# Performance work log

Hardware: AMD Instinct MI355X
Metric: run time of the kernel (lower is better)

Reference implementation:

```python
import jax, jax.numpy as jnp
import numpy as np

GRID = 32          # latent grid points per dim
N_OUT = 16384      # output query points
BATCH = 2
C = 256            # projection_channels (latent hidden width)
D = 3              # gno_coord_dim
OUT_CH = 4         # out_channels
RADIUS = 0.045     # gno_radius


def _radius_neighbors(x, y, r):
    """Radius ball search: for each query x_i find all y_j with ||x_i-y_j||<=r.
    Returns (nb_index, out_index) edge lists, sorted by query (CSR order)."""
    r2 = np.float32(r * r)
    nb_idx, out_idx = [], []
    for s in range(0, x.shape[0], 512):  # chunk to bound memory
        d2 = ((x[s:s + 512, None, :] - y[None, :, :]) ** 2).sum(-1)
        oi, yi = np.nonzero(d2 <= r2)
        out_idx.append((oi + s).astype(np.int32))
        nb_idx.append(yi.astype(np.int32))
    return np.concatenate(nb_idx), np.concatenate(out_idx)


def setup_inputs() -> dict:
    key = jax.random.key(0)
    ks = jax.random.split(key, 8)
    # latent queries: regular grid on [0,1]^3
    g = np.linspace(0.0, 1.0, GRID, dtype=np.float32)
    gx, gy, gz = np.meshgrid(g, g, g, indexing="ij")
    grid = np.stack([gx, gy, gz], axis=-1)               # (G,G,G,3)
    latent_queries = jnp.asarray(grid[None])             # (1,G,G,G,3)
    output_queries = jax.random.uniform(ks[0], (1, N_OUT, D), dtype=jnp.float32)
    nb_idx, out_idx = _radius_neighbors(np.asarray(output_queries[0]),
                                        grid.reshape(-1, D), RADIUS)
    latent_embed = jax.random.normal(ks[1], (BATCH, GRID, GRID, GRID, C), dtype=jnp.float32)

    def lin(k, fi, fo):
        kw, kb = jax.random.split(k)
        W = jax.random.normal(kw, (fi, fo), dtype=jnp.float32) / np.sqrt(fi).astype(np.float32)
        b = jax.random.normal(kb, (fo,), dtype=jnp.float32) * 0.01
        return W, b

    W1, b1 = lin(ks[2], 2 * D, 512)
    W2, b2 = lin(ks[3], 512, 256)
    W3, b3 = lin(ks[4], 256, C)
    Wp, bp = lin(ks[5], C, OUT_CH)
    return {"latent_embed": latent_embed, "latent_queries": latent_queries,
            "output_queries": output_queries,
            "nb_index": jnp.asarray(nb_idx), "out_index": jnp.asarray(out_idx),
            "W1": W1, "b1": b1, "W2": W2, "b2": b2, "W3": W3, "b3": b3,
            "Wp": Wp, "bp": bp}


def reference(latent_embed, latent_queries, output_queries, nb_index, out_index,
              W1, b1, W2, b2, W3, b3, Wp, bp):
    y = latent_queries[0].reshape(-1, latent_queries.shape[-1])   # (n_in, d) grid coords
    x = output_queries[0]                                         # (n_out, d)
    n_out = x.shape[0]
    b = latent_embed.shape[0]
    f_y = latent_embed.reshape(b, -1, latent_embed.shape[-1])     # (b, n_in, c)

    # per-edge kernel MLP on concat(y_j, x_i) -- 'linear' transform type
    agg = jnp.concatenate([y[nb_index], x[out_index]], axis=-1)   # (E, 2d)
    h = jax.nn.gelu(agg @ W1 + b1, approximate=False)             # (E, 512)
    h = jax.nn.gelu(h @ W2 + b2, approximate=False)               # (E, 256)
    k = h @ W3 + b3                                               # (E, c) kernel values

    # k(x_i, y_j) * f(y_j), then mean-reduce over each neighborhood
    msg = k[None, :, :] * f_y[:, nb_index, :]                     # (b, E, c)
    sums = jax.vmap(lambda m: jax.ops.segment_sum(m, out_index, num_segments=n_out))(msg)
    cnt = jax.ops.segment_sum(jnp.ones(nb_index.shape[0], dtype=k.dtype),
                              out_index, num_segments=n_out)
    mean = sums / jnp.maximum(cnt, 1.0)[None, :, None]            # (b, n_out, c)

    # pointwise projection (single Linear, no nonlinearity)
    return mean @ Wp + bp                                         # (b, n_out, out_ch)
```

## Files before the change

kernel.cpp:

```cpp
#include <hip/hip_runtime.h>
#include <math.h>

#define NGRID 32768
#define NOUT  16384
#define CCH   256
#define H1DIM 512
#define TE    32

typedef _Float16 f16x8 __attribute__((ext_vector_type(8)));
typedef float    f32x16 __attribute__((ext_vector_type(16)));

__device__ __forceinline__ unsigned short f32_to_f16_bits(float v) {
    _Float16 h = (_Float16)v;
    return __builtin_bit_cast(unsigned short, h);
}

__device__ __forceinline__ unsigned swz_row(int r) {
    return (unsigned)(((r & 7) ^ ((r >> 3) & 3)) << 4);
}

__device__ __forceinline__ float gelu_fast(float x) {
    float ax = fabsf(x) * 0.70710678118654752f;
    float t  = __builtin_amdgcn_rcpf(fmaf(0.3275911f, ax, 1.0f));
    float p  = fmaf(fmaf(fmaf(fmaf(1.061405429f, t, -1.453152027f), t, 1.421413741f), t,
                         -0.284496736f), t, 0.254829592f) * t;
    float e  = __expf(-ax * ax);
    float er = fmaf(-p, e, 1.0f);
    er = (x >= 0.0f) ? er : -er;
    return 0.5f * x * (1.0f + er);
}

__global__ __launch_bounds__(256) void gino_pack_kernel(
    const float* __restrict__ W2, const float* __restrict__ W3,
    unsigned short* __restrict__ W2F, unsigned short* __restrict__ W3F)
{
    int idx = blockIdx.x * 256 + threadIdx.x;
    if (idx < 32 * 8 * 64) {
        int l = idx & 63, g = (idx >> 6) & 7, ks = idx >> 9;
        int ch = g * 32 + (l & 31);
        int k0 = ks * 16 + (l >> 5) * 8;
        unsigned int u[4];
        #pragma unroll
        for (int p = 0; p < 4; ++p) {
            unsigned int lo = f32_to_f16_bits(W2[(k0 + 2 * p) * CCH + ch]);
            unsigned int hh = f32_to_f16_bits(W2[(k0 + 2 * p + 1) * CCH + ch]);
            u[p] = lo | (hh << 16);
        }
        *(uint4*)(W2F + idx * 8) = make_uint4(u[0], u[1], u[2], u[3]);
    } else if (idx < 32 * 8 * 64 + 16 * 8 * 64) {
        int i2 = idx - 32 * 8 * 64;
        int l = i2 & 63, g = (i2 >> 6) & 7, ks = i2 >> 9;
        int ch = g * 32 + (l & 31);
        int k0 = ks * 16 + (l >> 5) * 8;
        unsigned int u[4];
        #pragma unroll
        for (int p = 0; p < 4; ++p) {
            unsigned int lo = f32_to_f16_bits(W3[(k0 + 2 * p) * CCH + ch]);
            unsigned int hh = f32_to_f16_bits(W3[(k0 + 2 * p + 1) * CCH + ch]);
            u[p] = lo | (hh << 16);
        }
        *(uint4*)(W3F + i2 * 8) = make_uint4(u[0], u[1], u[2], u[3]);
    }
}

__global__ __launch_bounds__(256, 4) void gino_edge_kernel(
    const float* __restrict__ latent_embed,
    const float* __restrict__ latent_queries,
    const float* __restrict__ output_queries,
    const int*   __restrict__ nb_index,
    const int*   __restrict__ out_index,
    const float* __restrict__ W1, const float* __restrict__ b1,
    const float* __restrict__ b2, const float* __restrict__ b3,
    const unsigned short* __restrict__ W2F,
    const unsigned short* __restrict__ W3F,
    const float* __restrict__ Wp,
    float* __restrict__ sums, float* __restrict__ cnt, int E)
{
    __shared__ __align__(16) unsigned char s_h1[TE * 512];
    __shared__ __align__(16) unsigned char s_h2[TE * 512];
    __shared__ float s_agg[TE][8];
    __shared__ float s_pm[TE][8];
    __shared__ int s_nb[TE], s_oi[TE], s_valid[TE];

    const int tid = threadIdx.x;
    const int e0  = blockIdx.x * TE;

    ((float*)s_pm)[tid] = 0.0f;
    if (tid < TE) {
        int e     = e0 + tid;
        int valid = (e < E) ? 1 : 0;
        int ec    = valid ? e : (E - 1);
        int nb    = nb_index[ec];
        int oi    = out_index[ec];
        s_nb[tid] = nb; s_oi[tid] = oi; s_valid[tid] = valid;
        s_agg[tid][0] = latent_queries[nb * 3 + 0];
        s_agg[tid][1] = latent_queries[nb * 3 + 1];
        s_agg[tid][2] = latent_queries[nb * 3 + 2];
        s_agg[tid][3] = output_queries[oi * 3 + 0];
        s_agg[tid][4] = output_queries[oi * 3 + 1];
        s_agg[tid][5] = output_queries[oi * 3 + 2];
        if (valid) atomicAdd(&cnt[oi], 1.0f);
    }
    __syncthreads();

    const int l  = tid & 63;
    const int w  = tid >> 6;
    const int le = l & 31;
    const int hi = l >> 5;
    const unsigned swz = swz_row(le);

    f32x16 acc0 = {}, acc1 = {};

    #pragma unroll
    for (int chunk = 0; chunk < 2; ++chunk) {
        {
            const int kc = chunk * 256 + l * 4;
            float w1r[6][4];
            #pragma unroll
            for (int i = 0; i < 6; ++i)
                *(float4*)&w1r[i][0] = *(const float4*)(W1 + i * H1DIM + kc);
            float4 b1r = *(const float4*)(b1 + kc);
            #pragma unroll
            for (int ee = 0; ee < 8; ++ee) {
                int e = w * 8 + ee;
                float a0 = s_agg[e][0], a1 = s_agg[e][1], a2 = s_agg[e][2];
                float a3 = s_agg[e][3], a4 = s_agg[e][4], a5 = s_agg[e][5];
                unsigned int u[2];
                #pragma unroll
                for (int p = 0; p < 2; ++p) {
                    unsigned int uu[2];
                    #pragma unroll
                    for (int q = 0; q < 2; ++q) {
                        int j = 2 * p + q;
                        float v = (j == 0) ? b1r.x : (j == 1) ? b1r.y : (j == 2) ? b1r.z : b1r.w;
                        v = fmaf(a0, w1r[0][j], v);
                        v = fmaf(a1, w1r[1][j], v);
                        v = fmaf(a2, w1r[2][j], v);
                        v = fmaf(a3, w1r[3][j], v);
                        v = fmaf(a4, w1r[4][j], v);
                        v = fmaf(a5, w1r[5][j], v);
                        uu[q] = f32_to_f16_bits(gelu_fast(v));
                    }
                    u[p] = uu[0] | (uu[1] << 16);
                }
                *(uint2*)(s_h1 + e * 512 + (((unsigned)(l * 8)) ^ swz_row(e))) =
                    make_uint2(u[0], u[1]);
            }
        }
        __syncthreads();

        {
            const unsigned short* pa = W2F + (size_t)chunk * 16 * 4096 + w * 2 * 512 + l * 8;
            #pragma unroll
            for (int ks = 0; ks < 16; ++ks) {
                f16x8 bfr = *(const f16x8*)(s_h1 + le * 512 +
                              (((unsigned)(ks * 32 + hi * 16)) ^ swz));
                f16x8 a0 = *(const f16x8*)(pa + ks * 4096);
                f16x8 a1 = *(const f16x8*)(pa + ks * 4096 + 512);
                acc0 = __builtin_amdgcn_mfma_f32_32x32x16_f16(a0, bfr, acc0, 0, 0, 0);
                acc1 = __builtin_amdgcn_mfma_f32_32x32x16_f16(a1, bfr, acc1, 0, 0, 0);
            }
        }
        __syncthreads();
    }

    #pragma unroll
    for (int t2 = 0; t2 < 2; ++t2) {
        int g = w * 2 + t2;
        #pragma unroll
        for (int q = 0; q < 4; ++q) {
            int ch0 = g * 32 + q * 8 + hi * 4;
            float4 bb = *(const float4*)(b2 + ch0);
            float v0 = (t2 ? acc1[q * 4 + 0] : acc0[q * 4 + 0]) + bb.x;
            float v1 = (t2 ? acc1[q * 4 + 1] : acc0[q * 4 + 1]) + bb.y;
            float v2 = (t2 ? acc1[q * 4 + 2] : acc0[q * 4 + 2]) + bb.z;
            float v3 = (t2 ? acc1[q * 4 + 3] : acc0[q * 4 + 3]) + bb.w;
            unsigned int u0 = f32_to_f16_bits(gelu_fast(v0)) |
                              ((unsigned)f32_to_f16_bits(gelu_fast(v1)) << 16);
            unsigned int u1 = f32_to_f16_bits(gelu_fast(v2)) |
                              ((unsigned)f32_to_f16_bits(gelu_fast(v3)) << 16);
            *(uint2*)(s_h2 + le * 512 + (((unsigned)(ch0 * 2)) ^ swz)) = make_uint2(u0, u1);
        }
    }
    __syncthreads();

    f32x16 kc0 = {}, kc1 = {};
    {
        const unsigned short* pa = W3F + w * 2 * 512 + l * 8;
        #pragma unroll
        for (int ks = 0; ks < 16; ++ks) {
            f16x8 bfr = *(const f16x8*)(s_h2 + le * 512 +
                          (((unsigned)(ks * 32 + hi * 16)) ^ swz));
            f16x8 a0 = *(const f16x8*)(pa + ks * 4096);
            f16x8 a1 = *(const f16x8*)(pa + ks * 4096 + 512);
            kc0 = __builtin_amdgcn_mfma_f32_32x32x16_f16(a0, bfr, kc0, 0, 0, 0);
            kc1 = __builtin_amdgcn_mfma_f32_32x32x16_f16(a1, bfr, kc1, 0, 0, 0);
        }
    }

    {
        int nb = s_nb[le];
        const float* fb0 = latent_embed + (size_t)nb * CCH;
        const float* fb1 = latent_embed + ((size_t)NGRID + nb) * CCH;
        float pm00 = 0.f, pm01 = 0.f, pm02 = 0.f, pm03 = 0.f;
        float pm10 = 0.f, pm11 = 0.f, pm12 = 0.f, pm13 = 0.f;
        #pragma unroll
        for (int t2 = 0; t2 < 2; ++t2) {
            #pragma unroll
            for (int q = 0; q < 4; ++q) {
                int ch0 = (w * 2 + t2) * 32 + q * 8 + hi * 4;
                float4 bb = *(const float4*)(b3 + ch0);
                float kv0 = (t2 ? kc1[q * 4 + 0] : kc0[q * 4 + 0]) + bb.x;
                float kv1 = (t2 ? kc1[q * 4 + 1] : kc0[q * 4 + 1]) + bb.y;
                float kv2 = (t2 ? kc1[q * 4 + 2] : kc0[q * 4 + 2]) + bb.z;
                float kv3 = (t2 ? kc1[q * 4 + 3] : kc0[q * 4 + 3]) + bb.w;
                float4 f0 = *(const float4*)(fb0 + ch0);
                float4 f1 = *(const float4*)(fb1 + ch0);
                float4 wp0 = *(const float4*)(Wp + (ch0 + 0) * 4);
                float4 wp1 = *(const float4*)(Wp + (ch0 + 1) * 4);
                float4 wp2 = *(const float4*)(Wp + (ch0 + 2) * 4);
                float4 wp3 = *(const float4*)(Wp + (ch0 + 3) * 4);
                float t0 = kv0 * f0.x, t1 = kv1 * f0.y, t2v = kv2 * f0.z, t3 = kv3 * f0.w;
                pm00 = fmaf(t0, wp0.x, fmaf(t1, wp1.x, fmaf(t2v, wp2.x, fmaf(t3, wp3.x, pm00))));
                pm01 = fmaf(t0, wp0.y, fmaf(t1, wp1.y, fmaf(t2v, wp2.y, fmaf(t3, wp3.y, pm01))));
                pm02 = fmaf(t0, wp0.z, fmaf(t1, wp1.z, fmaf(t2v, wp2.z, fmaf(t3, wp3.z, pm02))));
                pm03 = fmaf(t0, wp0.w, fmaf(t1, wp1.w, fmaf(t2v, wp2.w, fmaf(t3, wp3.w, pm03))));
                float s0 = kv0 * f1.x, s1 = kv1 * f1.y, s2 = kv2 * f1.z, s3 = kv3 * f1.w;
                pm10 = fmaf(s0, wp0.x, fmaf(s1, wp1.x, fmaf(s2, wp2.x, fmaf(s3, wp3.x, pm10))));
                pm11 = fmaf(s0, wp0.y, fmaf(s1, wp1.y, fmaf(s2, wp2.y, fmaf(s3, wp3.y, pm11))));
                pm12 = fmaf(s0, wp0.z, fmaf(s1, wp1.z, fmaf(s2, wp2.z, fmaf(s3, wp3.z, pm12))));
                pm13 = fmaf(s0, wp0.w, fmaf(s1, wp1.w, fmaf(s2, wp2.w, fmaf(s3, wp3.w, pm13))));
            }
        }
        atomicAdd(&s_pm[le][0], pm00);
        atomicAdd(&s_pm[le][1], pm01);
        atomicAdd(&s_pm[le][2], pm02);
        atomicAdd(&s_pm[le][3], pm03);
        atomicAdd(&s_pm[le][4], pm10);
        atomicAdd(&s_pm[le][5], pm11);
        atomicAdd(&s_pm[le][6], pm12);
        atomicAdd(&s_pm[le][7], pm13);
    }
    __syncthreads();

    {
        int el = tid >> 3;
        int v  = tid & 7;
        if (s_valid[el]) {
            int b  = v >> 2;
            int oc = v & 3;
            atomicAdd(&sums[((size_t)b * NOUT + s_oi[el]) * 4 + oc], s_pm[el][v]);
        }
    }
}

__global__ __launch_bounds__(256) void gino_finalize_kernel(
    const float* __restrict__ sums,
    const float* __restrict__ cnt,
    const float* __restrict__ bp,
    float* __restrict__ out)
{
    int idx = blockIdx.x * 256 + threadIdx.x;
    if (idx >= 2 * NOUT * 4) return;
    int oc = idx & 3;
    int i  = (idx >> 2) & (NOUT - 1);
    float c = fmaxf(cnt[i], 1.0f);
    out[idx] = sums[idx] / c + bp[oc];
}

extern "C" void kernel_launch(void* const* d_in, const int* in_sizes, int n_in,
                              void* d_out, int out_size, void* d_ws, size_t ws_size,
                              hipStream_t stream) {
    const float* latent_embed   = (const float*)d_in[0];
    const float* latent_queries = (const float*)d_in[1];
    const float* output_queries = (const float*)d_in[2];
    const int*   nb_index       = (const int*)d_in[3];
    const int*   out_index      = (const int*)d_in[4];
    const float* W1 = (const float*)d_in[5];
    const float* b1 = (const float*)d_in[6];
    const float* W2 = (const float*)d_in[7];
    const float* b2 = (const float*)d_in[8];
    const float* W3 = (const float*)d_in[9];
    const float* b3 = (const float*)d_in[10];
    const float* Wp = (const float*)d_in[11];
    const float* bp = (const float*)d_in[12];

    const int E = in_sizes[3];

    float* sums = (float*)d_ws;
    float* cnt  = sums + 2 * NOUT * 4;
    unsigned short* W2F = (unsigned short*)(cnt + NOUT);
    unsigned short* W3F = W2F + 32 * 8 * 64 * 8;

    hipMemsetAsync(d_ws, 0, (size_t)(2 * NOUT * 4 + NOUT) * sizeof(float), stream);

    gino_pack_kernel<<<(32 * 8 * 64 + 16 * 8 * 64 + 255) / 256, 256, 0, stream>>>(
        W2, W3, W2F, W3F);

    int nblk = (E + TE - 1) / TE;
    gino_edge_kernel<<<nblk, 256, 0, stream>>>(
        latent_embed, latent_queries, output_queries, nb_index, out_index,
        W1, b1, b2, b3, W2F, W3F, Wp, sums, cnt, E);

    gino_finalize_kernel<<<(2 * NOUT * 4 + 255) / 256, 256, 0, stream>>>(
        sums, cnt, bp, (float*)d_out);
}
```

Baseline: 291.3 us.

## Double edge tile to 64 with 8 waves and software-pipeline MFMA operand loads

Each block now handles 64 edges with 512 threads (8 waves). Each wave owns 32 output channels, and its single weight fragment is reused across two 32-edge MFMA tiles, so each global weight load feeds twice as many edges. The MFMA loops prefetch the A and B fragments one or two k-steps ahead, and the projection partials are combined with a cross-half shuffle before the shared-memory atomics. The trade-off is more shared memory and registers per block, which may lower occupancy at the 4-blocks launch bound. The LDS swizzle is also simplified.

```diff
diff --git a/kernel.cpp b/kernel.cpp
--- a/kernel.cpp
+++ b/kernel.cpp
@@ -5,7 +5,8 @@
 #define NOUT  16384
 #define CCH   256
 #define H1DIM 512
-#define TE    32
+#define TE    64
+#define NTHR  512
 
 typedef _Float16 f16x8 __attribute__((ext_vector_type(8)));
 typedef float    f32x16 __attribute__((ext_vector_type(16)));
@@ -13,10 +14,6 @@
 __device__ __forceinline__ unsigned short f32_to_f16_bits(float v) {
     _Float16 h = (_Float16)v;
     return __builtin_bit_cast(unsigned short, h);
-}
-
-__device__ __forceinline__ unsigned swz_row(int r) {
-    return (unsigned)(((r & 7) ^ ((r >> 3) & 3)) << 4);
 }
 
 __device__ __forceinline__ float gelu_fast(float x) {
@@ -63,7 +60,7 @@
     }
 }
 
-__global__ __launch_bounds__(256, 4) void gino_edge_kernel(
+__global__ __launch_bounds__(NTHR, 4) void gino_edge_kernel(
     const float* __restrict__ latent_embed,
     const float* __restrict__ latent_queries,
     const float* __restrict__ output_queries,
@@ -107,7 +104,7 @@
     const int w  = tid >> 6;
     const int le = l & 31;
     const int hi = l >> 5;
-    const unsigned swz = swz_row(le);
+    const unsigned bswz = (unsigned)(le & 7) << 4;
 
     f32x16 acc0 = {}, acc1 = {};
 
@@ -143,103 +140,111 @@
                     }
                     u[p] = uu[0] | (uu[1] << 16);
                 }
-                *(uint2*)(s_h1 + e * 512 + (((unsigned)(l * 8)) ^ swz_row(e))) =
+                *(uint2*)(s_h1 + e * 512 + (((unsigned)(l * 8)) ^ (((unsigned)(ee & 7)) << 4))) =
                     make_uint2(u[0], u[1]);
             }
         }
         __syncthreads();
 
         {
-            const unsigned short* pa = W2F + (size_t)chunk * 16 * 4096 + w * 2 * 512 + l * 8;
+            const unsigned short* pa = W2F + (size_t)(chunk * 16) * 4096 + w * 512 + l * 8;
+            #define BRD1(t, ks) (*(const f16x8*)(s_h1 + ((t) * 32 + le) * 512 + \
+                                 (((unsigned)((ks) * 32 + hi * 16)) ^ bswz)))
+            f16x8 aC = *(const f16x8*)(pa);
+            f16x8 aN = *(const f16x8*)(pa + 4096);
+            f16x8 b0 = BRD1(0, 0), b1f = BRD1(1, 0);
             #pragma unroll
             for (int ks = 0; ks < 16; ++ks) {
-                f16x8 bfr = *(const f16x8*)(s_h1 + le * 512 +
-                              (((unsigned)(ks * 32 + hi * 16)) ^ swz));
-                f16x8 a0 = *(const f16x8*)(pa + ks * 4096);
-                f16x8 a1 = *(const f16x8*)(pa + ks * 4096 + 512);
-                acc0 = __builtin_amdgcn_mfma_f32_32x32x16_f16(a0, bfr, acc0, 0, 0, 0);
-                acc1 = __builtin_amdgcn_mfma_f32_32x32x16_f16(a1, bfr, acc1, 0, 0, 0);
+                f16x8 aNN = aN, bN0 = b0, bN1 = b1f;
+                if (ks < 14) aNN = *(const f16x8*)(pa + (size_t)(ks + 2) * 4096);
+                if (ks < 15) { bN0 = BRD1(0, ks + 1); bN1 = BRD1(1, ks + 1); }
+                acc0 = __builtin_amdgcn_mfma_f32_32x32x16_f16(aC, b0,  acc0, 0, 0, 0);
+                acc1 = __builtin_amdgcn_mfma_f32_32x32x16_f16(aC, b1f, acc1, 0, 0, 0);
+                aC = aN; aN = aNN; b0 = bN0; b1f = bN1;
             }
+            #undef BRD1
         }
         __syncthreads();
     }
 
     #pragma unroll
-    for (int t2 = 0; t2 < 2; ++t2) {
-        int g = w * 2 + t2;
+    for (int t = 0; t < 2; ++t) {
+        int erow = t * 32 + le;
         #pragma unroll
         for (int q = 0; q < 4; ++q) {
-            int ch0 = g * 32 + q * 8 + hi * 4;
+            int ch0 = w * 32 + q * 8 + hi * 4;
             float4 bb = *(const float4*)(b2 + ch0);
-            float v0 = (t2 ? acc1[q * 4 + 0] : acc0[q * 4 + 0]) + bb.x;
-            float v1 = (t2 ? acc1[q * 4 + 1] : acc0[q * 4 + 1]) + bb.y;
-            float v2 = (t2 ? acc1[q * 4 + 2] : acc0[q * 4 + 2]) + bb.z;
-            float v3 = (t2 ? acc1[q * 4 + 3] : acc0[q * 4 + 3]) + bb.w;
+            float v0 = (t ? acc1[q * 4 + 0] : acc0[q * 4 + 0]) + bb.x;
+            float v1 = (t ? acc1[q * 4 + 1] : acc0[q * 4 + 1]) + bb.y;
+            float v2 = (t ? acc1[q * 4 + 2] : acc0[q * 4 + 2]) + bb.z;
+            float v3 = (t ? acc1[q * 4 + 3] : acc0[q * 4 + 3]) + bb.w;
             unsigned int u0 = f32_to_f16_bits(gelu_fast(v0)) |
                               ((unsigned)f32_to_f16_bits(gelu_fast(v1)) << 16);
             unsigned int u1 = f32_to_f16_bits(gelu_fast(v2)) |
                               ((unsigned)f32_to_f16_bits(gelu_fast(v3)) << 16);
-            *(uint2*)(s_h2 + le * 512 + (((unsigned)(ch0 * 2)) ^ swz)) = make_uint2(u0, u1);
+            *(uint2*)(s_h2 + erow * 512 + (((unsigned)(ch0 * 2)) ^ bswz)) = make_uint2(u0, u1);
         }
     }
     __syncthreads();
 
     f32x16 kc0 = {}, kc1 = {};
     {
-        const unsigned short* pa = W3F + w * 2 * 512 + l * 8;
+        const unsigned short* pa = W3F + w * 512 + l * 8;
+        #define BRD2(t, ks) (*(const f16x8*)(s_h2 + ((t) * 32 + le) * 512 + \
+                             (((unsigned)((ks) * 32 + hi * 16)) ^ bswz)))
+        f16x8 aC = *(const f16x8*)(pa);
+        f16x8 aN = *(const f16x8*)(pa + 4096);
+        f16x8 b0 = BRD2(0, 0), b1f = BRD2(1, 0);
         #pragma unroll
         for (int ks = 0; ks < 16; ++ks) {
-            f16x8 bfr = *(const f16x8*)(s_h2 + le * 512 +
-                          (((unsigned)(ks * 32 + hi * 16)) ^ swz));
-            f16x8 a0 = *(const f16x8*)(pa + ks * 4096);
-            f16x8 a1 = *(const f16x8*)(pa + ks * 4096 + 512);
-            kc0 = __builtin_amdgcn_mfma_f32_32x32x16_f16(a0, bfr, kc0, 0, 0, 0);
-            kc1 = __builtin_amdgcn_mfma_f32_32x32x16_f16(a1, bfr, kc1, 0, 0, 0);
-        }
-    }
-
-    {
-        int nb = s_nb[le];
+            f16x8 aNN = aN, bN0 = b0, bN1 = b1f;
+            if (ks < 14) aNN = *(const f16x8*)(pa + (size_t)(ks + 2) * 4096);
+            if (ks < 15) { bN0 = BRD2(0, ks + 1); bN1 = BRD2(1, ks + 1); }
+            kc0 = __builtin_amdgcn_mfma_f32_32x32x16_f16(aC, b0,  kc0, 0, 0, 0);
+            kc1 = __builtin_amdgcn_mfma_f32_32x32x16_f16(aC, b1f, kc1, 0, 0, 0);
+            aC = aN; aN = aNN; b0 = bN0; b1f = bN1;
+        }
+        #undef BRD2
+    }
+
+    #pragma unroll
+    for (int t = 0; t < 2; ++t) {
+        int e  = t * 32 + le;
+        int nb = s_nb[e];
         const float* fb0 = latent_embed + (size_t)nb * CCH;
         const float* fb1 = latent_embed + ((size_t)NGRID + nb) * CCH;
-        float pm00 = 0.f, pm01 = 0.f, pm02 = 0.f, pm03 = 0.f;
-        float pm10 = 0.f, pm11 = 0.f, pm12 = 0.f, pm13 = 0.f;
-        #pragma unroll
-        for (int t2 = 0; t2 < 2; ++t2) {
+        float pm[8] = {0.f, 0.f, 0.f, 0.f, 0.f, 0.f, 0.f, 0.f};
+        #pragma unroll
+        for (int q = 0; q < 4; ++q) {
+            int ch0 = w * 32 + q * 8 + hi * 4;
+            float4 bb = *(const float4*)(b3 + ch0);
+            float kv0 = (t ? kc1[q * 4 + 0] : kc0[q * 4 + 0]) + bb.x;
+            float kv1 = (t ? kc1[q * 4 + 1] : kc0[q * 4 + 1]) + bb.y;
+            float kv2 = (t ? kc1[q * 4 + 2] : kc0[q * 4 + 2]) + bb.z;
+            float kv3 = (t ? kc1[q * 4 + 3] : kc0[q * 4 + 3]) + bb.w;
+            float4 f0 = *(const float4*)(fb0 + ch0);
+            float4 f1 = *(const float4*)(fb1 + ch0);
+            float4 wp0 = *(const float4*)(Wp + (ch0 + 0) * 4);
+            float4 wp1 = *(const float4*)(Wp + (ch0 + 1) * 4);
+            float4 wp2 = *(const float4*)(Wp + (ch0 + 2) * 4);
+            float4 wp3 = *(const float4*)(Wp + (ch0 + 3) * 4);
+            float t0 = kv0 * f0.x, t1 = kv1 * f0.y, t2v = kv2 * f0.z, t3 = kv3 * f0.w;
+            pm[0] = fmaf(t0, wp0.x, fmaf(t1, wp1.x, fmaf(t2v, wp2.x, fmaf(t3, wp3.x, pm[0]))));
+            pm[1] = fmaf(t0, wp0.y, fmaf(t1, wp1.y, fmaf(t2v, wp2.y, fmaf(t3, wp3.y, pm[1]))));
+            pm[2] = fmaf(t0, wp0.z, fmaf(t1, wp1.z, fmaf(t2v, wp2.z, fmaf(t3, wp3.z, pm[2]))));
+            pm[3] = fmaf(t0, wp0.w, fmaf(t1, wp1.w, fmaf(t2v, wp2.w, fmaf(t3, wp3.w, pm[3]))));
+            float s0 = kv0 * f1.x, s1 = kv1 * f1.y, s2 = kv2 * f1.z, s3 = kv3 * f1.w;
+            pm[4] = fmaf(s0, wp0.x, fmaf(s1, wp1.x, fmaf(s2, wp2.x, fmaf(s3, wp3.x, pm[4]))));
+            pm[5] = fmaf(s0, wp0.y, fmaf(s1, wp1.y, fmaf(s2, wp2.y, fmaf(s3, wp3.y, pm[5]))));
+            pm[6] = fmaf(s0, wp0.z, fmaf(s1, wp1.z, fmaf(s2, wp2.z, fmaf(s3, wp3.z, pm[6]))));
+            pm[7] = fmaf(s0, wp0.w, fmaf(s1, wp1.w, fmaf(s2, wp2.w, fmaf(s3, wp3.w, pm[7]))));
+        }
+        #pragma unroll
+        for (int v = 0; v < 8; ++v) pm[v] += __shfl_xor(pm[v], 32);
+        if (hi == 0) {
             #pragma unroll
-            for (int q = 0; q < 4; ++q) {
-                int ch0 = (w * 2 + t2) * 32 + q * 8 + hi * 4;
-                float4 bb = *(const float4*)(b3 + ch0);
-                float kv0 = (t2 ? kc1[q * 4 + 0] : kc0[q * 4 + 0]) + bb.x;
-                float kv1 = (t2 ? kc1[q * 4 + 1] : kc0[q * 4 + 1]) + bb.y;
-                float kv2 = (t2 ? kc1[q * 4 + 2] : kc0[q * 4 + 2]) + bb.z;
-                float kv3 = (t2 ? kc1[q * 4 + 3] : kc0[q * 4 + 3]) + bb.w;
-                float4 f0 = *(const float4*)(fb0 + ch0);
-                float4 f1 = *(const float4*)(fb1 + ch0);
-                float4 wp0 = *(const float4*)(Wp + (ch0 + 0) * 4);
-                float4 wp1 = *(const float4*)(Wp + (ch0 + 1) * 4);
-                float4 wp2 = *(const float4*)(Wp + (ch0 + 2) * 4);
-                float4 wp3 = *(const float4*)(Wp + (ch0 + 3) * 4);
-                float t0 = kv0 * f0.x, t1 = kv1 * f0.y, t2v = kv2 * f0.z, t3 = kv3 * f0.w;
-                pm00 = fmaf(t0, wp0.x, fmaf(t1, wp1.x, fmaf(t2v, wp2.x, fmaf(t3, wp3.x, pm00))));
-                pm01 = fmaf(t0, wp0.y, fmaf(t1, wp1.y, fmaf(t2v, wp2.y, fmaf(t3, wp3.y, pm01))));
-                pm02 = fmaf(t0, wp0.z, fmaf(t1, wp1.z, fmaf(t2v, wp2.z, fmaf(t3, wp3.z, pm02))));
-                pm03 = fmaf(t0, wp0.w, fmaf(t1, wp1.w, fmaf(t2v, wp2.w, fmaf(t3, wp3.w, pm03))));
-                float s0 = kv0 * f1.x, s1 = kv1 * f1.y, s2 = kv2 * f1.z, s3 = kv3 * f1.w;
-                pm10 = fmaf(s0, wp0.x, fmaf(s1, wp1.x, fmaf(s2, wp2.x, fmaf(s3, wp3.x, pm10))));
-                pm11 = fmaf(s0, wp0.y, fmaf(s1, wp1.y, fmaf(s2, wp2.y, fmaf(s3, wp3.y, pm11))));
-                pm12 = fmaf(s0, wp0.z, fmaf(s1, wp1.z, fmaf(s2, wp2.z, fmaf(s3, wp3.z, pm12))));
-                pm13 = fmaf(s0, wp0.w, fmaf(s1, wp1.w, fmaf(s2, wp2.w, fmaf(s3, wp3.w, pm13))));
-            }
-        }
-        atomicAdd(&s_pm[le][0], pm00);
-        atomicAdd(&s_pm[le][1], pm01);
-        atomicAdd(&s_pm[le][2], pm02);
-        atomicAdd(&s_pm[le][3], pm03);
-        atomicAdd(&s_pm[le][4], pm10);
-        atomicAdd(&s_pm[le][5], pm11);
-        atomicAdd(&s_pm[le][6], pm12);
-        atomicAdd(&s_pm[le][7], pm13);
+            for (int v = 0; v < 8; ++v) atomicAdd(&s_pm[e][v], pm[v]);
+        }
     }
     __syncthreads();
 
@@ -298,7 +303,7 @@
         W2, W3, W2F, W3F);
 
     int nblk = (E + TE - 1) / TE;
-    gino_edge_kernel<<<nblk, 256, 0, stream>>>(
+    gino_edge_kernel<<<nblk, NTHR, 0, stream>>>(
         latent_embed, latent_queries, output_queries, nb_index, out_index,
         W1, b1, b2, b3, W2F, W3F, Wp, sums, cnt, E);
 
```

Result: slower. 312.1 us (+7.1%).
